# Kernel optimization log

Measured on AMD Instinct MI355X. Metric: run time of the kernel, lower is better.

## Reference

```python
import jax, jax.numpy as jnp
import numpy as np

BLOCK_SIZE = 16
THRESH = 0.1


def _hadamard(n: int) -> np.ndarray:
    # Sylvester construction, matches WHTBlock.generate_walsh_matrix
    H = np.ones((1, 1), dtype=np.float32)
    while H.shape[0] < n:
        H = np.block([[H, H], [H, -H]])
    return H.astype(np.float32)


def setup_inputs() -> dict:
    key = jax.random.key(0)
    x = jax.random.normal(key, (32, 3, 1024, 1024), dtype=jnp.float32)
    return {"input": x}


def reference(input) -> jnp.ndarray:
    b, c, h, w = input.shape
    bs = BLOCK_SIZE
    # reflect-pad H, W up to a multiple of block_size (no-op when divisible)
    h_pad = (h + bs - 1) // bs * bs - h
    w_pad = (w + bs - 1) // bs * bs - w
    x = jnp.pad(input, ((0, 0), (0, 0), (0, h_pad), (0, w_pad)), mode="reflect")
    hn, wn = x.shape[-2:]
    # unfold into non-overlapping blocks: [b, c, nh, nw, bs, bs]
    x = x.reshape(b, c, hn // bs, bs, wn // bs, bs).transpose(0, 1, 2, 4, 3, 5)
    # normalized Hadamard: H / sqrt(n)
    Hn = jnp.asarray(_hadamard(bs)) / np.sqrt(np.float32(bs))
    # 2D WHT = Hn @ block @ Hn.T (H is symmetric but we keep the transposes explicit)
    x = jnp.einsum("bcnmij,kj->bcnmik", x, Hn)   # rows of each block: x @ Hn.T
    x = jnp.einsum("li,bcnmij->bcnmlj", Hn, x)   # cols of each block: Hn @ x
    # threshold: zero small-magnitude coefficients
    out = jnp.where(jnp.abs(x) < THRESH, jnp.zeros((), x.dtype), x)
    return out
```

## Files before the change

### kernel.cpp

```cpp
#include <hip/hip_runtime.h>

#define THRESH 0.1f

__global__ __launch_bounds__(256) void wht16_kernel(const float* __restrict__ in,
                                                    float* __restrict__ out) {
    const int wave = (blockIdx.x << 2) + (threadIdx.x >> 6);
    const int lane = threadIdx.x & 63;
    const int s = wave & 3;
    const int i = (wave >> 2) & 63;
    const int p = wave >> 8;

    const float* src = in + (size_t)p * 1048576 + (size_t)(i * 16) * 1024
                          + s * 256 + lane * 4;

    float v[16][4];
#pragma unroll
    for (int r = 0; r < 16; ++r) {
        const float4 t = *reinterpret_cast<const float4*>(src + (size_t)r * 1024);
        v[r][0] = t.x; v[r][1] = t.y; v[r][2] = t.z; v[r][3] = t.w;
    }

#pragma unroll
    for (int m = 1; m < 16; m <<= 1) {
#pragma unroll
        for (int r = 0; r < 16; ++r) {
            if (!(r & m)) {
#pragma unroll
                for (int k = 0; k < 4; ++k) {
                    const float a = v[r][k];
                    const float b = v[r | m][k];
                    v[r][k]     = a + b;
                    v[r | m][k] = a - b;
                }
            }
        }
    }

#pragma unroll
    for (int r = 0; r < 16; ++r) {
        float a, b;
        a = v[r][0]; b = v[r][1]; v[r][0] = a + b; v[r][1] = a - b;
        a = v[r][2]; b = v[r][3]; v[r][2] = a + b; v[r][3] = a - b;
        a = v[r][0]; b = v[r][2]; v[r][0] = a + b; v[r][2] = a - b;
        a = v[r][1]; b = v[r][3]; v[r][1] = a + b; v[r][3] = a - b;
    }

    const float s1 = (lane & 1) ? -1.0f : 1.0f;
    const float s2 = (lane & 2) ? -1.0f : 1.0f;
#pragma unroll
    for (int r = 0; r < 16; ++r) {
#pragma unroll
        for (int k = 0; k < 4; ++k) {
            const float pa = __shfl_xor(v[r][k], 1, 64);
            v[r][k] = fmaf(s1, v[r][k], pa);
        }
    }
#pragma unroll
    for (int r = 0; r < 16; ++r) {
#pragma unroll
        for (int k = 0; k < 4; ++k) {
            const float pa = __shfl_xor(v[r][k], 2, 64);
            v[r][k] = fmaf(s2, v[r][k], pa);
        }
    }

    const int j = (s << 4) + (lane >> 2);
    float4* dst = reinterpret_cast<float4*>(out)
                + ((size_t)((p * 64 + i) * 64 + j) << 6) + (lane & 3);
#pragma unroll
    for (int r = 0; r < 16; ++r) {
        float4 o;
        float x;
        x = v[r][0] * 0.0625f; o.x = (fabsf(x) < THRESH) ? 0.0f : x;
        x = v[r][1] * 0.0625f; o.y = (fabsf(x) < THRESH) ? 0.0f : x;
        x = v[r][2] * 0.0625f; o.z = (fabsf(x) < THRESH) ? 0.0f : x;
        x = v[r][3] * 0.0625f; o.w = (fabsf(x) < THRESH) ? 0.0f : x;
        dst[r * 4] = o;
    }
}

extern "C" void kernel_launch(void* const* d_in, const int* in_sizes, int n_in,
                              void* d_out, int out_size, void* d_ws, size_t ws_size,
                              hipStream_t stream) {
    const float* in = (const float*)d_in[0];
    float* out = (float*)d_out;
    const int blocks = 6144;
    wht16_kernel<<<blocks, 256, 0, stream>>>(in, out);
}
```

Baseline: 640.3 us.

## Split each 16x16 block row-pairs across lanes to double wave count

Each wave now processes 8 WHT blocks instead of 16, with even/odd row pairs assigned to different lane groups and combined by an extra xor-4 shuffle stage. Per-thread registers drop from 64 to 32 floats and the grid doubles, aiming to raise occupancy and memory-level parallelism in this bandwidth-bound kernel. The cost is extra cross-lane shuffles and a different store pattern. Grid size is now derived from the input size.

```diff
diff --git a/kernel.cpp b/kernel.cpp
--- a/kernel.cpp
+++ b/kernel.cpp
@@ -6,76 +6,89 @@
                                                     float* __restrict__ out) {
     const int wave = (blockIdx.x << 2) + (threadIdx.x >> 6);
     const int lane = threadIdx.x & 63;
-    const int s = wave & 3;
-    const int i = (wave >> 2) & 63;
-    const int p = wave >> 8;
 
-    const float* src = in + (size_t)p * 1048576 + (size_t)(i * 16) * 1024
-                          + s * 256 + lane * 4;
+    const int s8 = wave & 7;
+    const int i  = (wave >> 3) & 63;
+    const int p  = wave >> 9;
 
-    float v[16][4];
+    const int b   = lane >> 3;
+    const int par = (lane >> 2) & 1;
+    const int cg  = lane & 3;
+
+    const float* src = in + (size_t)p * 1048576
+                     + (size_t)(i * 16 + par) * 1024
+                     + s8 * 128 + b * 16 + cg * 4;
+
+    float v[8][4];
 #pragma unroll
-    for (int r = 0; r < 16; ++r) {
-        const float4 t = *reinterpret_cast<const float4*>(src + (size_t)r * 1024);
-        v[r][0] = t.x; v[r][1] = t.y; v[r][2] = t.z; v[r][3] = t.w;
+    for (int q = 0; q < 8; ++q) {
+        const float4 t = *reinterpret_cast<const float4*>(src + (size_t)q * 2048);
+        v[q][0] = t.x; v[q][1] = t.y; v[q][2] = t.z; v[q][3] = t.w;
     }
 
+    const float sp = par ? -1.0f : 1.0f;
 #pragma unroll
-    for (int m = 1; m < 16; m <<= 1) {
+    for (int q = 0; q < 8; ++q)
 #pragma unroll
-        for (int r = 0; r < 16; ++r) {
-            if (!(r & m)) {
+        for (int k = 0; k < 4; ++k) {
+            const float pa = __shfl_xor(v[q][k], 4, 64);
+            v[q][k] = fmaf(sp, v[q][k], pa);
+        }
+
+#pragma unroll
+    for (int mm = 1; mm < 8; mm <<= 1) {
+#pragma unroll
+        for (int q = 0; q < 8; ++q) {
+            if (!(q & mm)) {
 #pragma unroll
                 for (int k = 0; k < 4; ++k) {
-                    const float a = v[r][k];
-                    const float b = v[r | m][k];
-                    v[r][k]     = a + b;
-                    v[r | m][k] = a - b;
+                    const float a = v[q][k];
+                    const float c = v[q | mm][k];
+                    v[q][k]      = a + c;
+                    v[q | mm][k] = a - c;
                 }
             }
         }
     }
 
 #pragma unroll
-    for (int r = 0; r < 16; ++r) {
-        float a, b;
-        a = v[r][0]; b = v[r][1]; v[r][0] = a + b; v[r][1] = a - b;
-        a = v[r][2]; b = v[r][3]; v[r][2] = a + b; v[r][3] = a - b;
-        a = v[r][0]; b = v[r][2]; v[r][0] = a + b; v[r][2] = a - b;
-        a = v[r][1]; b = v[r][3]; v[r][1] = a + b; v[r][3] = a - b;
+    for (int q = 0; q < 8; ++q) {
+        float a, c;
+        a = v[q][0]; c = v[q][1]; v[q][0] = a + c; v[q][1] = a - c;
+        a = v[q][2]; c = v[q][3]; v[q][2] = a + c; v[q][3] = a - c;
+        a = v[q][0]; c = v[q][2]; v[q][0] = a + c; v[q][2] = a - c;
+        a = v[q][1]; c = v[q][3]; v[q][1] = a + c; v[q][3] = a - c;
     }
 
     const float s1 = (lane & 1) ? -1.0f : 1.0f;
     const float s2 = (lane & 2) ? -1.0f : 1.0f;
 #pragma unroll
-    for (int r = 0; r < 16; ++r) {
+    for (int q = 0; q < 8; ++q)
 #pragma unroll
         for (int k = 0; k < 4; ++k) {
-            const float pa = __shfl_xor(v[r][k], 1, 64);
-            v[r][k] = fmaf(s1, v[r][k], pa);
+            const float pa = __shfl_xor(v[q][k], 1, 64);
+            v[q][k] = fmaf(s1, v[q][k], pa);
         }
-    }
 #pragma unroll
-    for (int r = 0; r < 16; ++r) {
+    for (int q = 0; q < 8; ++q)
 #pragma unroll
         for (int k = 0; k < 4; ++k) {
-            const float pa = __shfl_xor(v[r][k], 2, 64);
-            v[r][k] = fmaf(s2, v[r][k], pa);
+            const float pa = __shfl_xor(v[q][k], 2, 64);
+            v[q][k] = fmaf(s2, v[q][k], pa);
         }
-    }
 
-    const int j = (s << 4) + (lane >> 2);
-    float4* dst = reinterpret_cast<float4*>(out)
-                + ((size_t)((p * 64 + i) * 64 + j) << 6) + (lane & 3);
+    const int j = s8 * 8 + b;
+    float* dst = out + ((size_t)((p * 64 + i) * 64 + j) << 8)
+               + par * 16 + cg * 4;
 #pragma unroll
-    for (int r = 0; r < 16; ++r) {
+    for (int q = 0; q < 8; ++q) {
         float4 o;
         float x;
-        x = v[r][0] * 0.0625f; o.x = (fabsf(x) < THRESH) ? 0.0f : x;
-        x = v[r][1] * 0.0625f; o.y = (fabsf(x) < THRESH) ? 0.0f : x;
-        x = v[r][2] * 0.0625f; o.z = (fabsf(x) < THRESH) ? 0.0f : x;
-        x = v[r][3] * 0.0625f; o.w = (fabsf(x) < THRESH) ? 0.0f : x;
-        dst[r * 4] = o;
+        x = v[q][0] * 0.0625f; o.x = (fabsf(x) < THRESH) ? 0.0f : x;
+        x = v[q][1] * 0.0625f; o.y = (fabsf(x) < THRESH) ? 0.0f : x;
+        x = v[q][2] * 0.0625f; o.z = (fabsf(x) < THRESH) ? 0.0f : x;
+        x = v[q][3] * 0.0625f; o.w = (fabsf(x) < THRESH) ? 0.0f : x;
+        *reinterpret_cast<float4*>(dst + q * 32) = o;
     }
 }
 
@@ -84,6 +97,7 @@
                               hipStream_t stream) {
     const float* in = (const float*)d_in[0];
     float* out = (float*)d_out;
-    const int blocks = 6144;
+    const long long n = (long long)in_sizes[0];
+    const int blocks = (int)(n / 8192);
     wht16_kernel<<<blocks, 256, 0, stream>>>(in, out);
 }
```

New measurement: 636.7 us. No clear change (-0.6%).
